# Kernel optimization log

Hardware: AMD Instinct MI355X
Metric: run time of the kernel (lower is better)

Reference implementation:

```python
import jax, jax.numpy as jnp
import numpy as np

B, N, D, E_PER, NT, ET, L = 32, 64, 128, 512, 32, 16, 6
E = B * E_PER


def _ln(y, g, b, eps=1e-5):
    m = jnp.mean(y, -1, keepdims=True)
    v = jnp.mean((y - m) ** 2, -1, keepdims=True)
    return (y - m) * jax.lax.rsqrt(v + eps) * g + b


def setup_inputs() -> dict:
    key = jax.random.key(0)
    ks = jax.random.split(key, 40)
    x = jax.random.randint(ks[0], (B * N,), 0, NT)
    src = jax.random.randint(ks[1], (E,), 0, N)
    dst = jax.random.randint(ks[2], (E,), 0, N)
    off = jnp.repeat(jnp.arange(B) * N, E_PER)
    edge_index = jnp.stack([src + off, dst + off])
    edge_attr = jax.random.randint(ks[3], (E,), 0, ET)
    t = jax.random.uniform(ks[4], (B,))

    def lin(k, fi, fo):
        return jax.random.normal(k, (fi, fo), jnp.float32) / np.sqrt(fi).astype(np.float32)

    inp = {
        'x': x, 'edge_index': edge_index, 'edge_attr': edge_attr, 't': t,
        'node_emb': (jax.random.normal(ks[5], (NT, D)) * 0.02).at[0].set(0.0),
        'edge_emb': (jax.random.normal(ks[6], (ET, D)) * 0.02).at[0].set(0.0),
        'temb_W1': lin(ks[7], 1, D), 'temb_b1': jnp.zeros(D),
        'temb_W2': lin(ks[8], D, D), 'temb_b2': jnp.zeros(D),
        'nin_W1': lin(ks[9], D, 2 * D), 'nin_b1': jnp.zeros(2 * D),
        'nin_W2': lin(ks[10], 2 * D, D), 'nin_b2': jnp.zeros(D),
        'ein_W1': lin(ks[11], D, 2 * D), 'ein_b1': jnp.zeros(2 * D),
        'ein_W2': lin(ks[12], 2 * D, D), 'ein_b2': jnp.zeros(D),
        'conv_W1': jax.random.normal(ks[13], (L, 3 * D, D)) / np.sqrt(3 * D).astype(np.float32),
        'conv_b1': jnp.zeros((L, D)),
        'conv_g1': jnp.ones((L, D)), 'conv_bt1': jnp.zeros((L, D)),
        'conv_W2': jax.random.normal(ks[14], (L, D, D)) / np.sqrt(D).astype(np.float32),
        'conv_b2': jnp.zeros((L, D)),
        'conv_g2': jnp.ones((L, D)), 'conv_bt2': jnp.zeros((L, D)),
        'mlp_W1': lin(ks[15], D, D), 'mlp_b1': jnp.zeros(D),
        'mlp_W2': lin(ks[16], D, D), 'mlp_b2': jnp.zeros(D),
        'fn_W1': lin(ks[17], D, 2 * D), 'fn_b1': jnp.zeros(2 * D),
        'fn_W2': lin(ks[18], 2 * D, D), 'fn_b2': jnp.zeros(D),
    }
    return inp


def reference(x, edge_index, edge_attr, t, node_emb, edge_emb,
              temb_W1, temb_b1, temb_W2, temb_b2,
              nin_W1, nin_b1, nin_W2, nin_b2,
              ein_W1, ein_b1, ein_W2, ein_b2,
              conv_W1, conv_b1, conv_g1, conv_bt1,
              conv_W2, conv_b2, conv_g2, conv_bt2,
              mlp_W1, mlp_b1, mlp_W2, mlp_b2,
              fn_W1, fn_b1, fn_W2, fn_b2):
    silu, relu = jax.nn.silu, jax.nn.relu
    # encoders
    h = node_emb[x]                                   # (B*N, D)
    e = edge_emb[edge_attr]                           # (E, D)
    h = relu(h @ nin_W1 + nin_b1) @ nin_W2 + nin_b2
    e = relu(e @ ein_W1 + ein_b1) @ ein_W2 + ein_b2
    # densify (to_dense_adj sums duplicate edges)
    g = edge_index[0] // N
    u = edge_index[0] % N
    v = edge_index[1] % N
    adj = jnp.zeros((B, N, N, D), h.dtype).at[g, u, v].add(e)
    # time embedding scales adj
    tt = silu(silu(t[:, None] @ temb_W1 + temb_b1) @ temb_W2 + temb_b2)  # (B, D)
    X = adj * tt[:, None, None, :]
    A = X  # A fixed to initial masked tensor, X updated residually
    for l in range(L):
        X1 = jnp.einsum('bikd,bkjd->bijd', A, X)      # aggregate over dim 1
        X2 = jnp.einsum('bikd,bkjd->bijd', X, A)      # aggregate over dim 2
        y = jnp.concatenate([X, X1, X2], -1)          # (B,N,N,3D)
        y = relu(_ln(y @ conv_W1[l] + conv_b1[l], conv_g1[l], conv_bt1[l]))
        y = relu(_ln(y @ conv_W2[l] + conv_b2[l], conv_g2[l], conv_bt2[l]))
        X = X + y                                     # residual, samesparse add
    X = X + jnp.transpose(X, (0, 2, 1, 3))
    e_out = X[g, u, v]                                # (E, D) edge gather
    h2 = (silu(X @ mlp_W1 + mlp_b1) @ mlp_W2 + mlp_b2).mean(-2).reshape(B * N, D)
    node_out = relu(h2 @ fn_W1 + fn_b1) @ fn_W2 + fn_b2
    edge_out = relu(e_out @ fn_W1 + fn_b1) @ fn_W2 + fn_b2  # original uses final_layer_node for edges too
    graph_attr = node_out.reshape(B, N, -1).mean(1)   # global mean pool
    return node_out, edge_out, graph_attr
```

## Files before the change

### kernel.cpp

```cpp
#include <hip/hip_runtime.h>
#include <hip/hip_bf16.h>
#include <math.h>

#define NB 32
#define NNODE 64
#define DD 128
#define NSQ 4096
#define EDGES 16384
#define LAYERS 6

typedef __bf16 bf16x8 __attribute__((ext_vector_type(8)));
typedef float f32x4 __attribute__((ext_vector_type(4)));

typedef __attribute__((address_space(1))) const unsigned int g_u32;
typedef __attribute__((address_space(3))) unsigned int l_u32;
__device__ __forceinline__ void gll16(const void* g, void* l){
  __builtin_amdgcn_global_load_lds((g_u32*)g, (l_u32*)l, 16, 0, 0);
}

__device__ __forceinline__ float silu_f(float x){ return x / (1.f + __expf(-x)); }
__device__ __forceinline__ float bf2f(unsigned short h){
  union{unsigned int u; float f;} x; x.u = ((unsigned int)h)<<16; return x.f;
}

__global__ void k_temb(const float* __restrict__ t, const float* __restrict__ W1,
                       const float* __restrict__ b1, const float* __restrict__ W2,
                       const float* __restrict__ b2, float* __restrict__ tt){
  int b = blockIdx.x, d = threadIdx.x;
  __shared__ float h[DD];
  float v = t[b]*W1[d] + b1[d];
  h[d] = silu_f(v);
  __syncthreads();
  float acc = b2[d];
  #pragma unroll 4
  for (int k=0;k<DD;k++) acc = fmaf(h[k], W2[k*DD+d], acc);
  tt[b*DD+d] = silu_f(acc);
}

__global__ void k_edgeenc(const float* __restrict__ emb, const float* __restrict__ W1,
                          const float* __restrict__ b1, const float* __restrict__ W2,
                          const float* __restrict__ b2, float* __restrict__ enc){
  int et = blockIdx.x, tid = threadIdx.x;
  __shared__ float e0[DD];
  __shared__ float hid[2*DD];
  if (tid < DD) e0[tid] = emb[et*DD + tid];
  __syncthreads();
  float a = b1[tid];
  for (int d2=0; d2<DD; d2++) a = fmaf(e0[d2], W1[d2*256 + tid], a);
  hid[tid] = fmaxf(a, 0.f);
  __syncthreads();
  if (tid < DD){
    float o = b2[tid];
    for (int k=0;k<256;k++) o = fmaf(hid[k], W2[k*DD + tid], o);
    enc[et*DD + tid] = o;
  }
}

__global__ void k_cnt(const int* __restrict__ ei, const int* __restrict__ attr,
                      unsigned int* __restrict__ cnt, int b0){
  int e = b0*512 + blockIdx.x*256 + threadIdx.x;
  int s = ei[e], dN = ei[EDGES+e];
  int g = (s>>6) - b0, u = s&63, v = dN&63;
  atomicAdd(&cnt[((size_t)g*4096 + v*64 + u)*16 + attr[e]], 1u);
}

__global__ __launch_bounds__(256) void k_expand(const unsigned int* __restrict__ cnt,
    const float* __restrict__ enc, const float* __restrict__ tt,
    __bf16* __restrict__ A_S, int b0){
  __shared__ float encs[16][128];
  __shared__ float ttl[128];
  __shared__ __bf16 tb[8][256];
  int g = blockIdx.x >> 4;
  int cell0 = (blockIdx.x & 15) << 8;
  int tid = threadIdx.x;
  for (int s = tid; s < 2048; s += 256) encs[s>>7][s&127] = enc[s];
  if (tid < 128) ttl[tid] = tt[(b0+g)*128 + tid];
  unsigned int c16[16];
  { const uint4* src = (const uint4*)(cnt + ((size_t)g*4096 + cell0 + tid)*16);
    uint4 a = src[0], b = src[1], c = src[2], d = src[3];
    c16[0]=a.x; c16[1]=a.y; c16[2]=a.z; c16[3]=a.w;
    c16[4]=b.x; c16[5]=b.y; c16[6]=b.z; c16[7]=b.w;
    c16[8]=c.x; c16[9]=c.y; c16[10]=c.z; c16[11]=c.w;
    c16[12]=d.x; c16[13]=d.y; c16[14]=d.z; c16[15]=d.w; }
  __syncthreads();
  for (int dc=0; dc<16; dc++){
    int d0 = dc*8;
    float vals[8] = {0.f,0.f,0.f,0.f,0.f,0.f,0.f,0.f};
    #pragma unroll
    for (int et=0; et<16; et++){
      unsigned int c = c16[et];
      if (c){
        float fc = (float)c;
        #pragma unroll
        for (int dd=0; dd<8; dd++) vals[dd] = fmaf(fc, encs[et][d0+dd], vals[dd]);
      }
    }
    #pragma unroll
    for (int dd=0; dd<8; dd++) tb[dd][tid] = (__bf16)(vals[dd]*ttl[d0+dd]);
    __syncthreads();
    { int dd = tid>>5, seg = tid&31;
      uint4 v = *(const uint4*)&tb[dd][seg*8];
      *(uint4*)(A_S + ((size_t)(g*128 + d0 + dd)<<12) + cell0 + seg*8) = v; }
    __syncthreads();
  }
}

__global__ __launch_bounds__(256) void k_wprep(const float* __restrict__ W1, const float* __restrict__ W2,
                                               const float* __restrict__ Wm, __bf16* __restrict__ WT){
  int b = blockIdx.x, t = threadIdx.x;
  const float* src; __bf16* dst; int K;
  if (b < 6){ src = W1 + (size_t)b*384*128; dst = WT + (size_t)b*49152; K = 384; }
  else if (b < 12){ src = W2 + (size_t)(b-6)*128*128; dst = WT + 294912 + (size_t)(b-6)*16384; K = 128; }
  else { src = Wm; dst = WT + 393216; K = 128; }
  __shared__ float L[64][129];
  for (int k0 = 0; k0 < K; k0 += 64){
    __syncthreads();
    int r = t>>2, c = (t&3)*32;
    #pragma unroll
    for (int e=0;e<32;e+=4){
      float4 x = *(const float4*)(src + (size_t)(k0+r)*128 + c + e);
      L[r][c+e]=x.x; L[r][c+e+1]=x.y; L[r][c+e+2]=x.z; L[r][c+e+3]=x.w;
    }
    __syncthreads();
    int fo = t>>1, kk = (t&1)*32;
    union { __bf16 h[32]; uint4 u[4]; } o;
    #pragma unroll
    for (int e=0;e<32;e++) o.h[e] = (__bf16)L[kk+e][fo];
    uint4* d4 = (uint4*)(dst + (size_t)fo*K + k0 + kk);
    d4[0]=o.u[0]; d4[1]=o.u[1]; d4[2]=o.u[2]; d4[3]=o.u[3];
  }
}

__global__ __launch_bounds__(256) void k_wprepfn(const float* __restrict__ W1, const float* __restrict__ W2,
                                                 __bf16* __restrict__ o1, __bf16* __restrict__ o2){
  int b = blockIdx.x, t = threadIdx.x;
  const float* src; __bf16* dst; int K, N, k0, n0;
  if (b < 8){ src = W1; dst = o1; K = 128; N = 256; k0 = (b>>2)*64; n0 = (b&3)*64; }
  else { int bb = b-8; src = W2; dst = o2; K = 256; N = 128; k0 = (bb>>1)*64; n0 = (bb&1)*64; }
  __shared__ float L[64][65];
  int r = t>>2, c4 = (t&3)*16;
  #pragma unroll
  for (int e=0;e<16;e+=4){
    float4 x = *(const float4*)(src + (size_t)(k0+r)*N + n0 + c4 + e);
    L[r][c4+e]=x.x; L[r][c4+e+1]=x.y; L[r][c4+e+2]=x.z; L[r][c4+e+3]=x.w;
  }
  __syncthreads();
  int n = t>>2, kc = (t&3)*16;
  union { __bf16 h[16]; uint4 u[2]; } o;
  #pragma unroll
  for (int e=0;e<16;e++) o.h[e] = (__bf16)L[kc+e][n];
  uint4* d4 = (uint4*)(dst + (size_t)(n0+n)*K + k0 + kc);
  d4[0]=o.u[0]; d4[1]=o.u[1];
}

__global__ __launch_bounds__(256) void k_einsum(const __bf16* __restrict__ As,
                                                const __bf16* __restrict__ Xs,
                                                __bf16* __restrict__ X1t, __bf16* __restrict__ X2t){
  __shared__ __bf16 S[8][4096];
  int tid = threadIdx.x;
  int w = tid>>6, lane = tid&63;
  size_t p0 = (size_t)blockIdx.x * 2;
  {
    int slot = (w<2) ? (2+w) : (4+w);
    const __bf16* srcp = ((w<2) ? As : Xs) + (p0 + (w&1))*4096;
    #pragma unroll
    for (int c8 = 0; c8 < 8; c8++){
      int row = c8*8 + (lane>>3);
      int ch  = (lane&7) ^ (row&7);
      gll16(srcp + row*64 + ch*8, (char*)&S[slot][0] + c8*1024);
    }
  }
  __syncthreads();
  {
    int q = tid>>6, v = tid&63;
    int ssl = (q<2) ? (2+q) : (4+q);
    int dsl = (q<2) ? q : (2+q);
    const unsigned char* sb = (const unsigned char*)S[ssl];
    unsigned char* db = (unsigned char*)S[dsl];
    #pragma unroll
    for (int uo=0; uo<8; uo++){
      union { __bf16 h[8]; uint4 u; } pk;
      #pragma unroll
      for (int e=0;e<8;e++){
        int u = uo*8+e;
        pk.h[e] = *(const __bf16*)(sb + u*128 + (((v>>3) ^ (u&7))<<4) + (v&7)*2);
      }
      *(uint4*)(db + v*128 + ((uo ^ (v&7))<<4)) = pk.u;
    }
  }
  __syncthreads();
  int pl = w>>1, pr = w&1;
  const __bf16* M  = pr ? S[4+pl] : S[0+pl];
  const __bf16* Bt = pr ? S[2+pl] : S[6+pl];
  f32x4 acc[4][4];
  #pragma unroll
  for (int a=0;a<4;a++)
    #pragma unroll
    for(int b=0;b<4;b++) acc[a][b] = (f32x4){0.f,0.f,0.f,0.f};
  int lr = lane&15, lq = lane>>4;
  #pragma unroll
  for (int ks=0;ks<2;ks++){
    bf16x8 af[4], bfr[4];
    #pragma unroll
    for (int mt=0;mt<4;mt++){ int r = mt*16+lr; af[mt] = *(const bf16x8*)&M[r*64 + (((ks*4+lq) ^ (r&7))<<3)]; }
    #pragma unroll
    for (int nt=0;nt<4;nt++){ int r = nt*16+lr; bfr[nt] = *(const bf16x8*)&Bt[r*64 + (((ks*4+lq) ^ (r&7))<<3)]; }
    #pragma unroll
    for (int mt=0;mt<4;mt++)
      #pragma unroll
      for (int nt=0;nt<4;nt++)
        acc[mt][nt] = __builtin_amdgcn_mfma_f32_16x16x32_bf16(af[mt], bfr[nt], acc[mt][nt], 0,0,0);
  }
  {
    int dslot = pr ? (4+pl) : pl;
    unsigned char* db = (unsigned char*)&S[dslot][0];
    #pragma unroll
    for (int mt=0;mt<4;mt++)
      #pragma unroll
      for (int nt=0;nt<4;nt++){
        int col = nt*16 + lr; int row0 = mt*16 + lq*4;
        union { __bf16 h[4]; uint2 u; } o;
        #pragma unroll
        for (int r=0;r<4;r++) o.h[r] = (__bf16)acc[mt][nt][r];
        int chunk = row0>>3;
        *(uint2*)(db + col*128 + ((chunk ^ (col&7))<<4) + (row0&7)*2) = o.u;
      }
  }
  __syncthreads();
  #pragma unroll
  for (int s4=0; s4<4; s4++){
    int slot = (s4<2) ? s4 : (2+s4);
    __bf16* dst = ((s4<2) ? X1t : X2t) + (p0 + (s4&1))*4096;
    const unsigned char* sb = (const unsigned char*)&S[slot][0];
    #pragma unroll
    for (int q=0;q<2;q++){
      int t2 = tid + q*256;
      int col = t2>>3, rc = t2&7;
      uint4 v = *(const uint4*)(sb + col*128 + ((rc ^ (col&7))<<4));
      *(uint4*)(dst + t2*8) = v;
    }
  }
}

__global__ __launch_bounds__(256) void k_layer(const __bf16* __restrict__ Xold,
    const __bf16* __restrict__ X1, const __bf16* __restrict__ X2,
    const __bf16* __restrict__ W1t, const __bf16* __restrict__ W2t,
    const float* __restrict__ b1v, const float* __restrict__ g1v, const float* __restrict__ bt1v,
    const float* __restrict__ b2v, const float* __restrict__ g2v, const float* __restrict__ bt2v,
    __bf16* __restrict__ Xnew){
  __shared__ __align__(16) unsigned char RG[32768];
  __shared__ float stats[2][128];
  unsigned char* Nc = RG;
  unsigned char* Cc = RG + 8192;
  __bf16* y1T = (__bf16*)RG;
  float (*redS)[128] = (float(*)[128])(RG + 16384);
  float (*redQ)[128] = (float(*)[128])(RG + 18432);
  int tid = threadIdx.x, w = tid>>6, lane = tid&63, lr = lane&15, lq = lane>>4;
  int colTile = blockIdx.x << 7;
  int bl = colTile >> 12;
  int colInB = colTile & 4095;
  int s_fi = tid>>3, s_o = tid&7;

  f32x4 acc[2][8];
  #pragma unroll
  for (int a=0;a<2;a++)
    #pragma unroll
    for (int b=0;b<8;b++) acc[a][b] = (f32x4){0.f,0.f,0.f,0.f};

  {
    int gfi = s_fi;
    const __bf16* T = Xold;
    const uint4* src = (const uint4*)(T + ((size_t)(bl*128 + gfi)<<12) + colInB + s_o*16);
    uint4 v0 = src[0], v1 = src[1];
    *(uint4*)(Nc + s_fi*256 + (((s_o*2+0) ^ (s_fi&15))<<4)) = v0;
    *(uint4*)(Nc + s_fi*256 + (((s_o*2+1) ^ (s_fi&15))<<4)) = v1;
  }
  __syncthreads();

  for (int ks=0; ks<12; ks++){
    { int col = tid>>1;
      #pragma unroll
      for (int j=0;j<2;j++){
        int oct = (tid&1)*2 + j;
        union { __bf16 h[8]; uint4 u; } pk;
        #pragma unroll
        for (int e=0;e<8;e++){
          int fi = oct*8 + e;
          pk.h[e] = *(const __bf16*)(Nc + fi*256 + (((col>>3) ^ (fi&15))<<4) + (col&7)*2);
        }
        *(uint4*)(Cc + col*64 + ((oct ^ (col&3))<<4)) = pk.u;
      }
    }
    __syncthreads();
    if (ks < 11){
      int gfi = (ks+1)*32 + s_fi;
      const __bf16* T = (gfi<128)? Xold : (gfi<256? X1 : X2);
      int d = gfi & 127;
      const uint4* src = (const uint4*)(T + ((size_t)(bl*128 + d)<<12) + colInB + s_o*16);
      uint4 v0 = src[0], v1 = src[1];
      *(uint4*)(Nc + s_fi*256 + (((s_o*2+0) ^ (s_fi&15))<<4)) = v0;
      *(uint4*)(Nc + s_fi*256 + (((s_o*2+1) ^ (s_fi&15))<<4)) = v1;
    }
    bf16x8 af[2];
    #pragma unroll
    for (int mt=0;mt<2;mt++){
      int fo = w*32 + mt*16 + lr;
      af[mt] = *(const bf16x8*)(W1t + (size_t)fo*384 + ks*32 + lq*8);
    }
    bf16x8 bfr[8];
    #pragma unroll
    for (int nt=0;nt<8;nt++){ int cr = nt*16+lr; bfr[nt] = *(const bf16x8*)(Cc + cr*64 + ((lq ^ (cr&3))<<4)); }
    #pragma unroll
    for (int mt=0;mt<2;mt++)
      #pragma unroll
      for (int nt=0;nt<8;nt++)
        acc[mt][nt] = __builtin_amdgcn_mfma_f32_16x16x32_bf16(af[mt], bfr[nt], acc[mt][nt], 0,0,0);
    __syncthreads();
  }

  #pragma unroll
  for (int mt=0;mt<2;mt++){
    #pragma unroll
    for (int r=0;r<4;r++){
      float bv = b1v[w*32 + mt*16 + lq*4 + r];
      #pragma unroll
      for (int nt=0;nt<8;nt++) acc[mt][nt][r] += bv;
    }
  }
  {
    float cs[8], cq[8];
    #pragma unroll
    for (int nt=0;nt<8;nt++){ cs[nt]=0.f; cq[nt]=0.f; }
    #pragma unroll
    for (int mt=0;mt<2;mt++)
      #pragma unroll
      for (int nt=0;nt<8;nt++)
        #pragma unroll
        for (int r=0;r<4;r++){ float v = acc[mt][nt][r]; cs[nt] += v; cq[nt] = fmaf(v,v,cq[nt]); }
    #pragma unroll
    for (int nt=0;nt<8;nt++){
      cs[nt] += __shfl_xor(cs[nt], 16); cq[nt] += __shfl_xor(cq[nt], 16);
      cs[nt] += __shfl_xor(cs[nt], 32); cq[nt] += __shfl_xor(cq[nt], 32);
    }
    if (lq == 0){
      #pragma unroll
      for (int nt=0;nt<8;nt++){ redS[w][nt*16+lr] = cs[nt]; redQ[w][nt*16+lr] = cq[nt]; }
    }
  }
  __syncthreads();
  if (tid < 128){
    float S = redS[0][tid]+redS[1][tid]+redS[2][tid]+redS[3][tid];
    float Q = redQ[0][tid]+redQ[1][tid]+redQ[2][tid]+redQ[3][tid];
    float m = S*(1.f/128.f);
    float var = Q*(1.f/128.f) - m*m;
    stats[0][tid] = m; stats[1][tid] = rsqrtf(var + 1e-5f);
  }
  __syncthreads();
  #pragma unroll
  for (int mt=0;mt<2;mt++){
    int fo1b = w*32 + mt*16 + lq*4;
    float ga[4], be[4];
    #pragma unroll
    for (int r=0;r<4;r++){ ga[r] = g1v[fo1b+r]; be[r] = bt1v[fo1b+r]; }
    #pragma unroll
    for (int nt=0;nt<8;nt++){
      int col = nt*16 + lr;
      union { __bf16 h[4]; uint2 u; } o;
      #pragma unroll
      for (int r=0;r<4;r++){
        float xx = (acc[mt][nt][r] - stats[0][col]) * stats[1][col] * ga[r] + be[r];
        o.h[r] = (__bf16)fmaxf(xx, 0.f);
      }
      *(uint2*)&y1T[col*128 + (fo1b ^ ((col&15)<<3))] = o.u;
    }
  }
  __syncthreads();

  f32x4 acc2[2][8];
  #pragma unroll
  for (int a=0;a<2;a++)
    #pragma unroll
    for (int b=0;b<8;b++) acc2[a][b] = (f32x4){0.f,0.f,0.f,0.f};
  #pragma unroll
  for (int ks2=0; ks2<4; ks2++){
    bf16x8 af[2], bfr[8];
    #pragma unroll
    for (int mt=0;mt<2;mt++){
      int fo = w*32 + mt*16 + lr;
      af[mt] = *(const bf16x8*)(W2t + (size_t)fo*128 + ks2*32 + lq*8);
    }
    #pragma unroll
    for (int nt=0;nt<8;nt++){ int cr = nt*16+lr; bfr[nt] = *(const bf16x8*)&y1T[cr*128 + ((ks2*32 + lq*8) ^ ((cr&15)<<3))]; }
    #pragma unroll
    for (int mt=0;mt<2;mt++)
      #pragma unroll
      for (int nt=0;nt<8;nt++)
        acc2[mt][nt] = __builtin_amdgcn_mfma_f32_16x16x32_bf16(af[mt], bfr[nt], acc2[mt][nt], 0,0,0);
  }
  __syncthreads();

  #pragma unroll
  for (int mt=0;mt<2;mt++){
    #pragma unroll
    for (int r=0;r<4;r++){
      float bv = b2v[w*32 + mt*16 + lq*4 + r];
      #pragma unroll
      for (int nt=0;nt<8;nt++) acc2[mt][nt][r] += bv;
    }
  }
  {
    float cs[8], cq[8];
    #pragma unroll
    for (int nt=0;nt<8;nt++){ cs[nt]=0.f; cq[nt]=0.f; }
    #pragma unroll
    for (int mt=0;mt<2;mt++)
      #pragma unroll
      for (int nt=0;nt<8;nt++)
        #pragma unroll
        for (int r=0;r<4;r++){ float v = acc2[mt][nt][r]; cs[nt] += v; cq[nt] = fmaf(v,v,cq[nt]); }
    #pragma unroll
    for (int nt=0;nt<8;nt++){
      cs[nt] += __shfl_xor(cs[nt], 16); cq[nt] += __shfl_xor(cq[nt], 16);
      cs[nt] += __shfl_xor(cs[nt], 32); cq[nt] += __shfl_xor(cq[nt], 32);
    }
    if (lq == 0){
      #pragma unroll
      for (int nt=0;nt<8;nt++){ redS[w][nt*16+lr] = cs[nt]; redQ[w][nt*16+lr] = cq[nt]; }
    }
  }
  __syncthreads();
  if (tid < 128){
    float S = redS[0][tid]+redS[1][tid]+redS[2][tid]+redS[3][tid];
    float Q = redQ[0][tid]+redQ[1][tid]+redQ[2][tid]+redQ[3][tid];
    float m = S*(1.f/128.f);
    float var = Q*(1.f/128.f) - m*m;
    stats[0][tid] = m; stats[1][tid] = rsqrtf(var + 1e-5f);
  }
  __syncthreads();
  #pragma unroll
  for (int mt=0;mt<2;mt++){
    #pragma unroll
    for (int r=0;r<4;r++){
      int fo = w*32 + mt*16 + lq*4 + r;
      float ga = g2v[fo], be = bt2v[fo];
      size_t rowb = ((size_t)(bl*128 + fo)<<12) + colInB;
      #pragma unroll
      for (int nt=0;nt<8;nt++){
        int cp = nt*16 + lr;
        float xx = (acc2[mt][nt][r] - stats[0][cp]) * stats[1][cp] * ga + be;
        float o = fmaxf(xx, 0.f);
        float old = (float)Xold[rowb + cp];
        Xnew[rowb + cp] = (__bf16)(o + old);
      }
    }
  }
}

__global__ __launch_bounds__(256) void k_sym(const __bf16* __restrict__ Xin, __bf16* __restrict__ Xout){
  __shared__ float P[64][65];
  size_t base = (size_t)blockIdx.x * 4096;
  int tid = threadIdx.x;
  int f = tid*16, r = f>>6, c = f&63;
  union { __bf16 h[16]; uint4 u[2]; } in;
  in.u[0] = *(const uint4*)(Xin + base + f);
  in.u[1] = *(const uint4*)(Xin + base + f + 8);
  #pragma unroll
  for (int e=0;e<16;e++) P[r][c+e] = (float)in.h[e];
  __syncthreads();
  union { __bf16 h[16]; uint4 u[2]; } o;
  #pragma unroll
  for (int e=0;e<16;e++) o.h[e] = (__bf16)(P[r][c+e] + P[c+e][r]);
  *(uint4*)(Xout + base + f)     = o.u[0];
  *(uint4*)(Xout + base + f + 8) = o.u[1];
}

__global__ __launch_bounds__(256) void k_tonm(const __bf16* __restrict__ S, __bf16* __restrict__ NM){
  __shared__ unsigned short L[64][65];
  int b = blockIdx.x;
  int g = b >> 7, dh = (b>>6)&1, cc = b&63;
  int cell0 = cc*64, d0 = dh*64;
  int tid = threadIdx.x;
  int r = tid>>2, c = (tid&3)*16;
  union { unsigned short h[16]; uint4 u[2]; } in;
  const unsigned short* src = (const unsigned short*)S + ((size_t)(g*128 + d0 + r)<<12) + cell0 + c;
  in.u[0] = *(const uint4*)src;
  in.u[1] = *(const uint4*)(src + 8);
  #pragma unroll
  for (int e=0;e<16;e++) L[r][c+e] = in.h[e];
  __syncthreads();
  union { unsigned short h[16]; uint4 u[2]; } o;
  int cr = tid>>2, dc = (tid&3)*16;
  #pragma unroll
  for (int e=0;e<16;e++) o.h[e] = L[dc+e][cr];
  unsigned short* dst = (unsigned short*)NM + (size_t)(g*4096 + cell0 + cr)*128 + d0 + dc;
  *(uint4*)dst       = o.u[0];
  *(uint4*)(dst + 8) = o.u[1];
}

__global__ __launch_bounds__(256) void k_mlph(const __bf16* __restrict__ NM,
    const __bf16* __restrict__ Wt, const float* __restrict__ bias, __bf16* __restrict__ hid){
  __shared__ __align__(16) unsigned char WcB[8192];
  __shared__ __align__(16) unsigned char EcB[8192];
  __bf16* Wc = (__bf16*)WcB;
  unsigned char* Ec = EcB;
  int tid = threadIdx.x, w = tid>>6, lane = tid&63, lr = lane&15, lq = lane>>4;
  int g = blockIdx.x >> 5;
  size_t cellbase = ((size_t)g<<12) + ((size_t)(blockIdx.x & 31) << 7);
  int mh = w&1, nh = w>>1;
  f32x4 acc[4][4];
  #pragma unroll
  for (int a=0;a<4;a++)
    #pragma unroll
    for (int b=0;b<4;b++) acc[a][b] = (f32x4){0.f,0.f,0.f,0.f};
  for (int ks=0; ks<4; ks++){
    __syncthreads();
    { int fo = tid>>1, half = tid&1;
      const uint4* src = (const uint4*)(Wt + (size_t)fo*128 + ks*32 + half*16);
      uint4 v0 = src[0], v1 = src[1];
      *(uint4*)&Wc[fo*32 + (((half*2+0) ^ (fo&3))<<3)] = v0;
      *(uint4*)&Wc[fo*32 + (((half*2+1) ^ (fo&3))<<3)] = v1;
    }
    { int cell = tid>>1, half = tid&1;
      const uint4* src = (const uint4*)(NM + (cellbase + cell)*128 + ks*32 + half*16);
      uint4 v0 = src[0], v1 = src[1];
      *(uint4*)(Ec + cell*64 + (((half*2+0) ^ (cell&3))<<4)) = v0;
      *(uint4*)(Ec + cell*64 + (((half*2+1) ^ (cell&3))<<4)) = v1;
    }
    __syncthreads();
    bf16x8 af[4], bfr[4];
    #pragma unroll
    for (int mt=0;mt<4;mt++){ int cr = mh*64 + mt*16 + lr; af[mt] = *(const bf16x8*)(Ec + cr*64 + ((lq ^ (cr&3))<<4)); }
    #pragma unroll
    for (int nt=0;nt<4;nt++){ int fo = nh*64 + nt*16 + lr; bfr[nt] = *(const bf16x8*)&Wc[fo*32 + ((lq ^ (fo&3))<<3)]; }
    #pragma unroll
    for (int mt=0;mt<4;mt++)
      #pragma unroll
      for (int nt=0;nt<4;nt++)
        acc[mt][nt] = __builtin_amdgcn_mfma_f32_16x16x32_bf16(af[mt], bfr[nt], acc[mt][nt], 0,0,0);
  }
  #pragma unroll
  for (int mt=0;mt<4;mt++)
    #pragma unroll
    for (int r=0;r<4;r++){
      size_t cell = cellbase + mh*64 + mt*16 + lq*4 + r;
      #pragma unroll
      for (int nt=0;nt<4;nt++){
        int fo = nh*64 + nt*16 + lr;
        hid[cell*128 + fo] = (__bf16)silu_f(acc[mt][nt][r] + bias[fo]);
      }
    }
}

__global__ void k_ymean(const __bf16* __restrict__ hid, float* __restrict__ ym){
  __shared__ float red[256];
  int g = blockIdx.x >> 6, u = blockIdx.x & 63;
  int fo = threadIdx.x & 127, vh = threadIdx.x >> 7;
  const unsigned short* hu = (const unsigned short*)hid;
  float s = 0.f;
  for (int v = vh; v < 64; v += 2)
    s += bf2f(hu[((size_t)g*4096 + v*64 + u)*128 + fo]);
  red[threadIdx.x] = s;
  __syncthreads();
  if (vh == 0) ym[((size_t)g*64 + u)*128 + fo] = (red[fo] + red[128+fo]) * (1.f/64.f);
}

__global__ void k_h2(const float* __restrict__ ym, const float* __restrict__ W2,
                     const float* __restrict__ b2, float* __restrict__ h2){
  int row = blockIdx.x, fo = threadIdx.x;
  __shared__ float rr[128];
  rr[fo] = ym[(size_t)row*128 + fo];
  __syncthreads();
  float a = b2[fo];
  #pragma unroll 4
  for (int k=0;k<128;k++) a = fmaf(rr[k], W2[k*128+fo], a);
  h2[(size_t)row*128+fo] = a;
}

template<int GATHER>
__global__ __launch_bounds__(256) void k_fmlp(const __bf16* __restrict__ NM, const float* __restrict__ RWS,
    const int* __restrict__ ei,
    const __bf16* __restrict__ W1t, const float* __restrict__ b1,
    const __bf16* __restrict__ W2t, const float* __restrict__ b2,
    float* __restrict__ outp, int b0){
  __shared__ __align__(16) unsigned char RA[32768];
  __shared__ __align__(16) unsigned char RB[8192];
  __shared__ int cells[64];
  __bf16* eo  = (__bf16*)RA;
  __bf16* Wc  = (__bf16*)(RA + 16384);
  __bf16* hid = (__bf16*)RA;
  __bf16* W2c = (__bf16*)RB;
  int tid = threadIdx.x, w = tid>>6, lane = tid&63, lr = lane&15, lq = lane>>4;
  int r0 = blockIdx.x*64;
  if (GATHER){
    if (tid < 64){
      int e = b0*512 + r0 + tid;
      int s = ei[e], dN = ei[EDGES+e];
      cells[tid] = ((s>>6) - b0)*4096 + (dN&63)*64 + (s&63);
    }
    __syncthreads();
  }
  { int el = tid>>2, o4 = tid&3;
    if (GATHER){
      const unsigned short* src = (const unsigned short*)NM + (size_t)cells[el]*128;
      #pragma unroll
      for (int j=0;j<4;j++){
        int ch = o4*4 + j;
        uint4 v = *(const uint4*)(src + ch*8);
        *(uint4*)&eo[el*128 + ((ch*8) ^ ((el&15)*8))] = v;
      }
    } else {
      const float* src = RWS + (size_t)(r0 + el)*128;
      #pragma unroll
      for (int j=0;j<4;j++){
        int ch = o4*4 + j;
        union { __bf16 h[8]; uint4 u; } pk;
        #pragma unroll
        for (int e2=0;e2<8;e2++) pk.h[e2] = (__bf16)src[ch*8 + e2];
        *(uint4*)&eo[el*128 + ((ch*8) ^ ((el&15)*8))] = pk.u;
      }
    }
  }
  f32x4 acc[4][4];
  #pragma unroll
  for (int a=0;a<4;a++)
    #pragma unroll
    for (int b=0;b<4;b++) acc[a][b] = (f32x4){0.f,0.f,0.f,0.f};
  for (int ks=0; ks<4; ks++){
    if (ks) __syncthreads();
    { int fo = tid;
      const uint4* src = (const uint4*)(W1t + (size_t)fo*128 + ks*32);
      #pragma unroll
      for (int o=0;o<4;o++){
        uint4 v = src[o];
        *(uint4*)&Wc[fo*32 + ((o ^ (fo&3))<<3)] = v;
      }
    }
    __syncthreads();
    bf16x8 af[4], bfr[4];
    #pragma unroll
    for (int mt=0;mt<4;mt++){ int fo = w*64+mt*16+lr; af[mt] = *(const bf16x8*)&Wc[fo*32 + ((lq ^ (fo&3))<<3)]; }
    #pragma unroll
    for (int nt=0;nt<4;nt++){ int ed = nt*16+lr; bfr[nt] = *(const bf16x8*)&eo[ed*128 + ((ks*32+lq*8) ^ ((ed&15)*8))]; }
    #pragma unroll
    for (int mt=0;mt<4;mt++)
      #pragma unroll
      for (int nt=0;nt<4;nt++)
        acc[mt][nt] = __builtin_amdgcn_mfma_f32_16x16x32_bf16(af[mt], bfr[nt], acc[mt][nt], 0,0,0);
  }
  __syncthreads();
  #pragma unroll
  for (int mt=0;mt<4;mt++){
    int fob = w*64 + mt*16 + lq*4;
    float bv[4];
    #pragma unroll
    for (int r=0;r<4;r++) bv[r] = b1[fob+r];
    #pragma unroll
    for (int nt=0;nt<4;nt++){
      int ed = nt*16 + lr;
      union { __bf16 h[4]; uint2 u; } o;
      #pragma unroll
      for (int r=0;r<4;r++) o.h[r] = (__bf16)fmaxf(acc[mt][nt][r] + bv[r], 0.f);
      *(uint2*)&hid[ed*256 + (fob ^ ((ed&31)*8))] = o.u;
    }
  }
  f32x4 acc2[4][2];
  #pragma unroll
  for (int a=0;a<4;a++)
    #pragma unroll
    for (int b=0;b<2;b++) acc2[a][b] = (f32x4){0.f,0.f,0.f,0.f};
  int mh = w&1, nh = w>>1;
  for (int ks2=0; ks2<8; ks2++){
    __syncthreads();
    { int fo = tid>>1, half = tid&1;
      const uint4* src = (const uint4*)(W2t + (size_t)fo*256 + ks2*32 + half*16);
      uint4 v0 = src[0], v1 = src[1];
      *(uint4*)&W2c[fo*32 + (((half*2+0) ^ (fo&3))<<3)] = v0;
      *(uint4*)&W2c[fo*32 + (((half*2+1) ^ (fo&3))<<3)] = v1;
    }
    __syncthreads();
    bf16x8 af2[4], bfr2[2];
    #pragma unroll
    for (int mt=0;mt<4;mt++){ int fo2 = mh*64+mt*16+lr; af2[mt] = *(const bf16x8*)&W2c[fo2*32 + ((lq ^ (fo2&3))<<3)]; }
    #pragma unroll
    for (int nt=0;nt<2;nt++){ int ed = nh*32+nt*16+lr; bfr2[nt] = *(const bf16x8*)&hid[ed*256 + ((ks2*32+lq*8) ^ ((ed&31)*8))]; }
    #pragma unroll
    for (int mt=0;mt<4;mt++)
      #pragma unroll
      for (int nt=0;nt<2;nt++)
        acc2[mt][nt] = __builtin_amdgcn_mfma_f32_16x16x32_bf16(af2[mt], bfr2[nt], acc2[mt][nt], 0,0,0);
  }
  #pragma unroll
  for (int mt=0;mt<4;mt++){
    int fo2b = mh*64 + mt*16 + lq*4;
    float bv[4];
    #pragma unroll
    for (int r=0;r<4;r++) bv[r] = b2[fo2b+r];
    #pragma unroll
    for (int nt=0;nt<2;nt++){
      int ed = nh*32 + nt*16 + lr;
      float4 o = make_float4(acc2[mt][nt][0]+bv[0], acc2[mt][nt][1]+bv[1],
                             acc2[mt][nt][2]+bv[2], acc2[mt][nt][3]+bv[3]);
      *(float4*)(outp + (size_t)(r0 + ed)*128 + fo2b) = o;
    }
  }
}

__global__ void k_graph(const float* __restrict__ node_out, float* __restrict__ gout){
  int b = blockIdx.x, d = threadIdx.x;
  float s = 0.f;
  for (int i=0;i<64;i++) s += node_out[(size_t)(b*64+i)*128 + d];
  gout[b*128 + d] = s * (1.f/64.f);
}

extern "C" void kernel_launch(void* const* d_in, const int* in_sizes, int n_in,
                              void* d_out, int out_size, void* d_ws, size_t ws_size,
                              hipStream_t stream) {
  const int*   edge_index = (const int*)d_in[1];
  const int*   edge_attr  = (const int*)d_in[2];
  const float* t        = (const float*)d_in[3];
  const float* edge_emb = (const float*)d_in[5];
  const float* temb_W1  = (const float*)d_in[6];
  const float* temb_b1  = (const float*)d_in[7];
  const float* temb_W2  = (const float*)d_in[8];
  const float* temb_b2  = (const float*)d_in[9];
  const float* ein_W1   = (const float*)d_in[14];
  const float* ein_b1   = (const float*)d_in[15];
  const float* ein_W2   = (const float*)d_in[16];
  const float* ein_b2   = (const float*)d_in[17];
  const float* conv_W1  = (const float*)d_in[18];
  const float* conv_b1  = (const float*)d_in[19];
  const float* conv_g1  = (const float*)d_in[20];
  const float* conv_bt1 = (const float*)d_in[21];
  const float* conv_W2  = (const float*)d_in[22];
  const float* conv_b2  = (const float*)d_in[23];
  const float* conv_g2  = (const float*)d_in[24];
  const float* conv_bt2 = (const float*)d_in[25];
  const float* mlp_W1   = (const float*)d_in[26];
  const float* mlp_b1   = (const float*)d_in[27];
  const float* mlp_W2   = (const float*)d_in[28];
  const float* mlp_b2   = (const float*)d_in[29];
  const float* fn_W1    = (const float*)d_in[30];
  const float* fn_b1    = (const float*)d_in[31];
  const float* fn_W2    = (const float*)d_in[32];
  const float* fn_b2    = (const float*)d_in[33];

  float* ws  = (float*)d_ws;
  float* tt  = ws;
  float* enc = ws + 4096;
  float* ym  = ws + 6144;
  float* h2  = ws + 268288;
  __bf16* WT = (__bf16*)(ws + 530432);
  unsigned int* cnt = (unsigned int*)(ws + 768000);
  const size_t HDRF = 2883584;

  __bf16* fnW1t = WT + 409600;
  __bf16* fnW2t = WT + 442368;

  size_t availF = ws_size / sizeof(float);
  const int cands[6] = {32, 16, 8, 4, 2, 1};
  int C = 1;
  for (int i = 0; i < 6; i++){
    if (HDRF + 4ull * (size_t)cands[i] * 262144ull <= availF){ C = cands[i]; break; }
  }
  const size_t PCB = (size_t)C * 262144;
  __bf16* A_S = (__bf16*)(ws + HDRF);
  __bf16* X_S = (__bf16*)(ws + HDRF + PCB);
  __bf16* X1  = (__bf16*)(ws + HDRF + 2*PCB);
  __bf16* X2  = (__bf16*)(ws + HDRF + 3*PCB);
  float* outf = (float*)d_out;

  k_temb<<<NB, DD, 0, stream>>>(t, temb_W1, temb_b1, temb_W2, temb_b2, tt);
  k_edgeenc<<<16, 256, 0, stream>>>(edge_emb, ein_W1, ein_b1, ein_W2, ein_b2, enc);
  k_wprep<<<13, 256, 0, stream>>>(conv_W1, conv_W2, mlp_W1, WT);
  k_wprepfn<<<16, 256, 0, stream>>>(fn_W1, fn_W2, fnW1t, fnW2t);

  for (int b0 = 0; b0 < NB; b0 += C){
    hipMemsetAsync(cnt, 0, (size_t)C*4096*16*sizeof(unsigned int), stream);
    k_cnt<<<C*2, 256, 0, stream>>>(edge_index, edge_attr, cnt, b0);
    k_expand<<<C*16, 256, 0, stream>>>(cnt, enc, tt, A_S, b0);

    for (int l=0; l<LAYERS; l++){
      const __bf16* Xs_l = (l==0) ? A_S : X_S;
      k_einsum<<<C*64, 256, 0, stream>>>(A_S, Xs_l, X1, X2);
      k_layer<<<C*32, 256, 0, stream>>>(Xs_l, X1, X2,
          WT + (size_t)l*49152, WT + 294912 + (size_t)l*16384,
          conv_b1 + l*DD, conv_g1 + l*DD, conv_bt1 + l*DD,
          conv_b2 + l*DD, conv_g2 + l*DD, conv_bt2 + l*DD, X_S);
    }

    k_sym<<<C*128, 256, 0, stream>>>(X_S, X2);
    k_tonm<<<C*128, 256, 0, stream>>>(X2, X1);
    k_mlph<<<C*32, 256, 0, stream>>>(X1, WT + 393216, mlp_b1, X2);
    k_ymean<<<C*64, 256, 0, stream>>>(X2, ym);
    k_h2<<<C*64, 128, 0, stream>>>(ym, mlp_W2, mlp_b2, h2);
    k_fmlp<1><<<C*8, 256, 0, stream>>>(X1, nullptr, edge_index, fnW1t, fn_b1, fnW2t, fn_b2,
                                       outf + 262144 + (size_t)b0*512*128, b0);
    k_fmlp<0><<<C, 256, 0, stream>>>(nullptr, h2, nullptr, fnW1t, fn_b1, fnW2t, fn_b2,
                                     outf + (size_t)b0*64*128, b0);
    k_graph<<<C, DD, 0, stream>>>(outf + (size_t)b0*64*DD, outf + 2359296 + b0*DD);
  }
}
```

Measured before the change: 599.2 us.

## Double-buffer k_layer operand staging and fuse mean reduction into MLP kernel

The first GEMM loop in k_layer now uses two staging buffers and two repacked buffers in shared memory. The global load and repack for the next K-slice are issued after the current MFMA step, which leaves one barrier per iteration instead of two. Separately, k_mlph no longer writes the bf16 hidden tensor. It atomically adds silu outputs scaled by 1/64 straight into a zeroed fp32 ym buffer, so the k_ymean kernel and its reread of the hidden tensor go away. The cost is heavy float atomic traffic, and a summation order that is no longer deterministic.

```diff
diff --git a/kernel.cpp b/kernel.cpp
--- a/kernel.cpp
+++ b/kernel.cpp
@@ -250,8 +250,6 @@
     __bf16* __restrict__ Xnew){
   __shared__ __align__(16) unsigned char RG[32768];
   __shared__ float stats[2][128];
-  unsigned char* Nc = RG;
-  unsigned char* Cc = RG + 8192;
   __bf16* y1T = (__bf16*)RG;
   float (*redS)[128] = (float(*)[128])(RG + 16384);
   float (*redQ)[128] = (float(*)[128])(RG + 18432);
@@ -260,6 +258,7 @@
   int bl = colTile >> 12;
   int colInB = colTile & 4095;
   int s_fi = tid>>3, s_o = tid&7;
+  int r_col = tid>>1;
 
   f32x4 acc[2][8];
   #pragma unroll
@@ -267,45 +266,47 @@
     #pragma unroll
     for (int b=0;b<8;b++) acc[a][b] = (f32x4){0.f,0.f,0.f,0.f};
 
-  {
-    int gfi = s_fi;
-    const __bf16* T = Xold;
-    const uint4* src = (const uint4*)(T + ((size_t)(bl*128 + gfi)<<12) + colInB + s_o*16);
-    uint4 v0 = src[0], v1 = src[1];
-    *(uint4*)(Nc + s_fi*256 + (((s_o*2+0) ^ (s_fi&15))<<4)) = v0;
-    *(uint4*)(Nc + s_fi*256 + (((s_o*2+1) ^ (s_fi&15))<<4)) = v1;
-  }
-  __syncthreads();
-
-  for (int ks=0; ks<12; ks++){
-    { int col = tid>>1;
-      #pragma unroll
-      for (int j=0;j<2;j++){
-        int oct = (tid&1)*2 + j;
-        union { __bf16 h[8]; uint4 u; } pk;
-        #pragma unroll
-        for (int e=0;e<8;e++){
-          int fi = oct*8 + e;
-          pk.h[e] = *(const __bf16*)(Nc + fi*256 + (((col>>3) ^ (fi&15))<<4) + (col&7)*2);
-        }
-        *(uint4*)(Cc + col*64 + ((oct ^ (col&3))<<4)) = pk.u;
-      }
-    }
-    __syncthreads();
-    if (ks < 11){
-      int gfi = (ks+1)*32 + s_fi;
-      const __bf16* T = (gfi<128)? Xold : (gfi<256? X1 : X2);
-      int d = gfi & 127;
-      const uint4* src = (const uint4*)(T + ((size_t)(bl*128 + d)<<12) + colInB + s_o*16);
-      uint4 v0 = src[0], v1 = src[1];
-      *(uint4*)(Nc + s_fi*256 + (((s_o*2+0) ^ (s_fi&15))<<4)) = v0;
-      *(uint4*)(Nc + s_fi*256 + (((s_o*2+1) ^ (s_fi&15))<<4)) = v1;
-    }
+#define STAGE(ks, nb) { \
+    int gfi = (ks)*32 + s_fi; \
+    const __bf16* T = (gfi<128)? Xold : (gfi<256? X1 : X2); \
+    int d = gfi & 127; \
+    const uint4* src = (const uint4*)(T + ((size_t)(bl*128 + d)<<12) + colInB + s_o*16); \
+    uint4 v0 = src[0], v1 = src[1]; \
+    unsigned char* Nd = RG + (nb)*8192; \
+    *(uint4*)(Nd + s_fi*256 + (((s_o*2+0) ^ (s_fi&15))<<4)) = v0; \
+    *(uint4*)(Nd + s_fi*256 + (((s_o*2+1) ^ (s_fi&15))<<4)) = v1; \
+  }
+
+#define REPACK(nb) { \
+    const unsigned char* Ns = RG + (nb)*8192; \
+    unsigned char* Cd = RG + 16384 + (nb)*8192; \
+    _Pragma("unroll") \
+    for (int j=0;j<2;j++){ \
+      int oct = (tid&1)*2 + j; \
+      union { __bf16 h[8]; uint4 u; } pk; \
+      _Pragma("unroll") \
+      for (int e=0;e<8;e++){ \
+        int fi = oct*8 + e; \
+        pk.h[e] = *(const __bf16*)(Ns + fi*256 + (((r_col>>3) ^ (fi&15))<<4) + (r_col&7)*2); \
+      } \
+      *(uint4*)(Cd + r_col*64 + ((oct ^ (r_col&3))<<4)) = pk.u; \
+    } \
+  }
+
+  STAGE(0, 0)
+  STAGE(1, 1)
+  __syncthreads();
+  REPACK(0)
+  __syncthreads();
+
+  for (int k=0; k<11; k++){
+    int cb = k&1, nb = cb^1;
+    const unsigned char* Cc = RG + 16384 + cb*8192;
     bf16x8 af[2];
     #pragma unroll
     for (int mt=0;mt<2;mt++){
       int fo = w*32 + mt*16 + lr;
-      af[mt] = *(const bf16x8*)(W1t + (size_t)fo*384 + ks*32 + lq*8);
+      af[mt] = *(const bf16x8*)(W1t + (size_t)fo*384 + k*32 + lq*8);
     }
     bf16x8 bfr[8];
     #pragma unroll
@@ -315,7 +316,26 @@
       #pragma unroll
       for (int nt=0;nt<8;nt++)
         acc[mt][nt] = __builtin_amdgcn_mfma_f32_16x16x32_bf16(af[mt], bfr[nt], acc[mt][nt], 0,0,0);
-    __syncthreads();
+    REPACK(nb)
+    if (k < 10) STAGE(k+2, cb)
+    __syncthreads();
+  }
+  {
+    const unsigned char* Cc = RG + 16384 + 8192;
+    bf16x8 af[2];
+    #pragma unroll
+    for (int mt=0;mt<2;mt++){
+      int fo = w*32 + mt*16 + lr;
+      af[mt] = *(const bf16x8*)(W1t + (size_t)fo*384 + 11*32 + lq*8);
+    }
+    bf16x8 bfr[8];
+    #pragma unroll
+    for (int nt=0;nt<8;nt++){ int cr = nt*16+lr; bfr[nt] = *(const bf16x8*)(Cc + cr*64 + ((lq ^ (cr&3))<<4)); }
+    #pragma unroll
+    for (int mt=0;mt<2;mt++)
+      #pragma unroll
+      for (int nt=0;nt<8;nt++)
+        acc[mt][nt] = __builtin_amdgcn_mfma_f32_16x16x32_bf16(af[mt], bfr[nt], acc[mt][nt], 0,0,0);
   }
 
   #pragma unroll
@@ -454,6 +474,8 @@
       }
     }
   }
+#undef STAGE
+#undef REPACK
 }
 
 __global__ __launch_bounds__(256) void k_sym(const __bf16* __restrict__ Xin, __bf16* __restrict__ Xout){
@@ -498,7 +520,7 @@
 }
 
 __global__ __launch_bounds__(256) void k_mlph(const __bf16* __restrict__ NM,
-    const __bf16* __restrict__ Wt, const float* __restrict__ bias, __bf16* __restrict__ hid){
+    const __bf16* __restrict__ Wt, const float* __restrict__ bias, float* __restrict__ ym){
   __shared__ __align__(16) unsigned char WcB[8192];
   __shared__ __align__(16) unsigned char EcB[8192];
   __bf16* Wc = (__bf16*)WcB;
@@ -542,26 +564,15 @@
   for (int mt=0;mt<4;mt++)
     #pragma unroll
     for (int r=0;r<4;r++){
-      size_t cell = cellbase + mh*64 + mt*16 + lq*4 + r;
+      int cc = mh*64 + mt*16 + lq*4 + r;
+      int u = cc & 63;
       #pragma unroll
       for (int nt=0;nt<4;nt++){
         int fo = nh*64 + nt*16 + lr;
-        hid[cell*128 + fo] = (__bf16)silu_f(acc[mt][nt][r] + bias[fo]);
+        atomicAdd(&ym[((size_t)g*64 + u)*128 + fo],
+                  silu_f(acc[mt][nt][r] + bias[fo]) * (1.f/64.f));
       }
     }
-}
-
-__global__ void k_ymean(const __bf16* __restrict__ hid, float* __restrict__ ym){
-  __shared__ float red[256];
-  int g = blockIdx.x >> 6, u = blockIdx.x & 63;
-  int fo = threadIdx.x & 127, vh = threadIdx.x >> 7;
-  const unsigned short* hu = (const unsigned short*)hid;
-  float s = 0.f;
-  for (int v = vh; v < 64; v += 2)
-    s += bf2f(hu[((size_t)g*4096 + v*64 + u)*128 + fo]);
-  red[threadIdx.x] = s;
-  __syncthreads();
-  if (vh == 0) ym[((size_t)g*64 + u)*128 + fo] = (red[fo] + red[128+fo]) * (1.f/64.f);
 }
 
 __global__ void k_h2(const float* __restrict__ ym, const float* __restrict__ W2,
@@ -790,8 +801,8 @@
 
     k_sym<<<C*128, 256, 0, stream>>>(X_S, X2);
     k_tonm<<<C*128, 256, 0, stream>>>(X2, X1);
-    k_mlph<<<C*32, 256, 0, stream>>>(X1, WT + 393216, mlp_b1, X2);
-    k_ymean<<<C*64, 256, 0, stream>>>(X2, ym);
+    hipMemsetAsync(ym, 0, (size_t)C*8192*sizeof(float), stream);
+    k_mlph<<<C*32, 256, 0, stream>>>(X1, WT + 393216, mlp_b1, ym);
     k_h2<<<C*64, 128, 0, stream>>>(ym, mlp_W2, mlp_b2, h2);
     k_fmlp<1><<<C*8, 256, 0, stream>>>(X1, nullptr, edge_index, fnW1t, fn_b1, fnW2t, fn_b2,
                                        outf + 262144 + (size_t)b0*512*128, b0);
```

New measurement: 626.0 us. 1.04x slower.
